# Optimization experiments

Hardware: AMD Instinct MI355X
Metric: run time of the kernel (lower is better)

Reference implementation:

```python
import jax, jax.numpy as jnp
import numpy as np

B, L, DIM = 2, 2048, 768
NH, HD = 12, 64  # num_heads, head_dim; NH*HD == dim_attn == 768


def setup_inputs() -> dict:
    key = jax.random.key(0)
    ks = jax.random.split(key, 7)
    x = jax.random.normal(ks[0], (B, L, DIM), dtype=jnp.float32)
    pos_bias = jax.random.normal(ks[1], (1, NH, L, L), dtype=jnp.float32)
    Wq = jax.random.normal(ks[2], (DIM, DIM), dtype=jnp.float32) * 0.02
    Wk = jax.random.normal(ks[3], (DIM, DIM), dtype=jnp.float32) * 0.02
    Wv = jax.random.normal(ks[4], (DIM, DIM), dtype=jnp.float32) * 0.02
    Wo = jax.random.normal(ks[5], (DIM, DIM), dtype=jnp.float32) * 0.02
    mask = jax.random.randint(ks[6], (B, L), 0, 2, dtype=jnp.int32)
    return {"x": x, "pos_bias": pos_bias, "Wq": Wq, "Wk": Wk, "Wv": Wv,
            "Wo": Wo, "mask": mask}


def reference(x, pos_bias, Wq, Wk, Wv, Wo, mask):
    b, l, _ = x.shape
    # q/k/v projections (torch Linear: x @ W.T), split into heads
    q = (x @ Wq.T).reshape(b, l, NH, HD)
    k = (x @ Wk.T).reshape(b, l, NH, HD)
    v = (x @ Wv.T).reshape(b, l, NH, HD)
    # additive bias [B, H, Lq, Lk]: pos_bias broadcast + key mask -> -inf
    neg_inf = jnp.finfo(x.dtype).min
    attn_bias = jnp.broadcast_to(pos_bias, (b, NH, l, l))
    attn_bias = jnp.where(mask[:, None, None, :] == 0, neg_inf, attn_bias)
    # T5-style attention: NO 1/sqrt(d) scaling
    scores = jnp.einsum('binc,bjnc->bnij', q, k) + attn_bias
    attn = jax.nn.softmax(scores.astype(jnp.float32), axis=-1).astype(x.dtype)
    out = jnp.einsum('bnij,bjnc->binc', attn, v).reshape(b, l, NH * HD)
    return out @ Wo.T
```

## Files before the change

kernel.cpp:

```cpp
#include <hip/hip_runtime.h>
#include <math.h>

#define Bq 2
#define Lq 2048
#define DIMq 768
#define NHq 12
#define HDq 64

typedef __attribute__((ext_vector_type(8))) short short8;
typedef __attribute__((ext_vector_type(4))) short short4v;
typedef __attribute__((ext_vector_type(4))) float float4v;

static __device__ __forceinline__ short f2bf(float f) {
    union { float f; unsigned u; } v; v.f = f;
    unsigned r = (v.u + 0x7FFF + ((v.u >> 16) & 1)) >> 16;
    return (short)r;
}

__global__ __launch_bounds__(256)
void to_bf16(const float* __restrict__ x,  const float* __restrict__ wq,
             const float* __restrict__ wk, const float* __restrict__ wv,
             const float* __restrict__ wo,
             short* __restrict__ xb, short* __restrict__ wqb,
             short* __restrict__ wkb, short* __restrict__ wvb,
             short* __restrict__ wob)
{
    int blk = blockIdx.x;
    const float* s; short* d; int off;
    if      (blk <  768) { s = x;  d = xb;  off = blk * 1024; }
    else if (blk <  912) { s = wq; d = wqb; off = (blk -  768) * 1024; }
    else if (blk < 1056) { s = wk; d = wkb; off = (blk -  912) * 1024; }
    else if (blk < 1200) { s = wv; d = wvb; off = (blk - 1056) * 1024; }
    else                 { s = wo; d = wob; off = (blk - 1200) * 1024; }
    const float4* s4 = (const float4*)s;
    short4v* d4 = (short4v*)d;
#pragma unroll
    for (int i = 0; i < 4; ++i) {
        int idx = off + threadIdx.x + i * 256;
        float4 v = s4[idx];
        short4v o;
        o[0] = f2bf(v.x); o[1] = f2bf(v.y); o[2] = f2bf(v.z); o[3] = f2bf(v.w);
        d4[idx] = o;
    }
}

__global__ __launch_bounds__(256, 2)
void gemm_bf16(const short* __restrict__ A,
               const short* __restrict__ W0, const short* __restrict__ W1,
               const short* __restrict__ W2,
               short* __restrict__ D0, short* __restrict__ D1,
               short* __restrict__ D2, float* __restrict__ DF, int mode)
{
    const int z = blockIdx.z;
    const short* W = (z == 0) ? W0 : ((z == 1) ? W1 : W2);
    short* DH = (z == 0) ? D0 : ((z == 1) ? D1 : D2);

    __shared__ __align__(16) short Xs[64][72];
    __shared__ __align__(16) short Ws[64][72];

    const int tid  = threadIdx.x;
    const int wave = tid >> 6;
    const int lane = tid & 63;
    const int col  = lane & 15;
    const int quad = lane >> 4;
    const int m0 = blockIdx.y * 64, n0 = blockIdx.x * 64;

    float4v acc[4];
#pragma unroll
    for (int nt = 0; nt < 4; ++nt) acc[nt] = (float4v){0.f, 0.f, 0.f, 0.f};

    for (int k0 = 0; k0 < DIMq; k0 += 64) {
        __syncthreads();
#pragma unroll
        for (int i = 0; i < 2; ++i) {
            int idx = tid + i * 256;
            int mm = idx >> 3, ch = idx & 7;
            *(short8*)&Xs[mm][ch * 8] =
                *(const short8*)&A[(size_t)(m0 + mm) * DIMq + k0 + ch * 8];
            *(short8*)&Ws[mm][ch * 8] =
                *(const short8*)&W[(size_t)(n0 + mm) * DIMq + k0 + ch * 8];
        }
        __syncthreads();
#pragma unroll
        for (int kk = 0; kk < 2; ++kk) {
            short8 a = *(const short8*)&Xs[wave * 16 + col][kk * 32 + quad * 8];
#pragma unroll
            for (int nt = 0; nt < 4; ++nt) {
                short8 bfr = *(const short8*)&Ws[nt * 16 + col][kk * 32 + quad * 8];
                acc[nt] = __builtin_amdgcn_mfma_f32_16x16x32_bf16(a, bfr, acc[nt], 0, 0, 0);
            }
        }
    }

#pragma unroll
    for (int reg = 0; reg < 4; ++reg) {
        int m = m0 + wave * 16 + quad * 4 + reg;
#pragma unroll
        for (int nt = 0; nt < 4; ++nt) {
            int n = n0 + 16 * nt + col;
            if (mode == 1) {
                int b = m >> 11, l = m & 2047, h = n >> 6, c = n & 63;
                DH[(((size_t)(b * NHq + h)) * Lq + l) * HDq + c] = f2bf(acc[nt][reg]);
            } else {
                DF[(size_t)m * DIMq + n] = acc[nt][reg];
            }
        }
    }
}

__global__ __launch_bounds__(256, 2)
void attn_fwd_mfma(const short* __restrict__ Qh, const short* __restrict__ Kh,
                   const short* __restrict__ Vh, const float* __restrict__ pos_bias,
                   const int* __restrict__ mask, short* __restrict__ AO)
{
    const int qt = blockIdx.x;
    const int h  = blockIdx.y;
    const int b  = blockIdx.z;
    const short* Q = Qh + ((size_t)(b * NHq + h)) * Lq * HDq;
    const short* K = Kh + ((size_t)(b * NHq + h)) * Lq * HDq;
    const short* V = Vh + ((size_t)(b * NHq + h)) * Lq * HDq;
    const int* mk = mask + (size_t)b * Lq;

    __shared__ __align__(16) short Ks[64][72];
    __shared__ __align__(16) short Vt[64][72];
    __shared__ __align__(16) short Ps[64][72];

    const int tid  = threadIdx.x;
    const int wave = tid >> 6;
    const int lane = tid & 63;
    const int col  = lane & 15;
    const int quad = lane >> 4;

    short8 qa[2];
    {
        const short* qrow = Q + (size_t)(qt * 64 + wave * 16 + col) * HDq;
        qa[0] = *(const short8*)&qrow[quad * 8];
        qa[1] = *(const short8*)&qrow[32 + quad * 8];
    }

    const float* brow = pos_bias + (size_t)h * Lq * Lq
                      + (size_t)(qt * 64 + wave * 16 + quad * 4) * Lq + col;

    float bcur[4][4], bnxt[4][4];
    auto prefetch = [&](int kt, float (&bb)[4][4]) {
#pragma unroll
        for (int nt = 0; nt < 4; ++nt) {
            int mval = mk[kt * 64 + col + 16 * nt];
            float fm = (mval == 0) ? -1e30f : 0.0f;
#pragma unroll
            for (int reg = 0; reg < 4; ++reg)
                bb[nt][reg] = brow[(size_t)reg * Lq + kt * 64 + 16 * nt] + fm;
        }
    };
    prefetch(0, bcur);

    float4v Oacc[4];
    float m_run[4], l_run[4];
#pragma unroll
    for (int nt = 0; nt < 4; ++nt) Oacc[nt] = (float4v){0.f, 0.f, 0.f, 0.f};
#pragma unroll
    for (int r = 0; r < 4; ++r) { m_run[r] = -1e30f; l_run[r] = 0.f; }

    for (int kt = 0; kt < Lq / 64; ++kt) {
        __syncthreads();
        const short* Kt = K + (size_t)kt * 64 * HDq;
        const short* Vg = V + (size_t)kt * 64 * HDq;
#pragma unroll
        for (int i = 0; i < 2; ++i) {
            int idx = tid + i * 256;
            int key = idx >> 3, ch = idx & 7;
            *(short8*)&Ks[key][ch * 8] = *(const short8*)&Kt[key * HDq + ch * 8];
        }
        {
            int key = tid & 63, hg = tid >> 6;
#pragma unroll
            for (int i = 0; i < 2; ++i) {
                int c = hg + i * 4;
                short8 vv = *(const short8*)&Vg[key * HDq + c * 8];
#pragma unroll
                for (int j = 0; j < 8; ++j)
                    Vt[c * 8 + j][key] = vv[j];
            }
        }
        if (kt + 1 < Lq / 64) prefetch(kt + 1, bnxt);
        __syncthreads();

        float4v S[4];
#pragma unroll
        for (int nt = 0; nt < 4; ++nt) S[nt] = (float4v){0.f, 0.f, 0.f, 0.f};
#pragma unroll
        for (int kk = 0; kk < 2; ++kk) {
#pragma unroll
            for (int nt = 0; nt < 4; ++nt) {
                short8 bfr = *(const short8*)&Ks[nt * 16 + col][kk * 32 + quad * 8];
                S[nt] = __builtin_amdgcn_mfma_f32_16x16x32_bf16(qa[kk], bfr, S[nt], 0, 0, 0);
            }
        }

        float sc[4][4];
#pragma unroll
        for (int nt = 0; nt < 4; ++nt)
#pragma unroll
            for (int reg = 0; reg < 4; ++reg)
                sc[nt][reg] = S[nt][reg] + bcur[nt][reg];
        float tm[4];
#pragma unroll
        for (int reg = 0; reg < 4; ++reg) {
            tm[reg] = fmaxf(fmaxf(sc[0][reg], sc[1][reg]),
                            fmaxf(sc[2][reg], sc[3][reg]));
#pragma unroll
            for (int off = 1; off < 16; off <<= 1)
                tm[reg] = fmaxf(tm[reg], __shfl_xor(tm[reg], off, 64));
        }
        float alpha[4], ps[4];
#pragma unroll
        for (int reg = 0; reg < 4; ++reg) {
            float mn = fmaxf(m_run[reg], tm[reg]);
            alpha[reg] = __expf(m_run[reg] - mn);
            m_run[reg] = mn;
            ps[reg] = 0.f;
        }
#pragma unroll
        for (int nt = 0; nt < 4; ++nt)
#pragma unroll
            for (int reg = 0; reg < 4; ++reg) {
                float p = __expf(sc[nt][reg] - m_run[reg]);
                sc[nt][reg] = p;
                ps[reg] += p;
            }
#pragma unroll
        for (int reg = 0; reg < 4; ++reg) {
#pragma unroll
            for (int off = 1; off < 16; off <<= 1)
                ps[reg] += __shfl_xor(ps[reg], off, 64);
            l_run[reg] = l_run[reg] * alpha[reg] + ps[reg];
        }
#pragma unroll
        for (int nt = 0; nt < 4; ++nt)
#pragma unroll
            for (int reg = 0; reg < 4; ++reg)
                Ps[wave * 16 + quad * 4 + reg][col + 16 * nt] = f2bf(sc[nt][reg]);
#pragma unroll
        for (int nt = 0; nt < 4; ++nt)
#pragma unroll
            for (int reg = 0; reg < 4; ++reg)
                Oacc[nt][reg] *= alpha[reg];
        __syncthreads();

#pragma unroll
        for (int kk = 0; kk < 2; ++kk) {
            short8 pa = *(const short8*)&Ps[wave * 16 + col][kk * 32 + quad * 8];
#pragma unroll
            for (int nt = 0; nt < 4; ++nt) {
                short8 vb = *(const short8*)&Vt[nt * 16 + col][kk * 32 + quad * 8];
                Oacc[nt] = __builtin_amdgcn_mfma_f32_16x16x32_bf16(pa, vb, Oacc[nt], 0, 0, 0);
            }
        }
#pragma unroll
        for (int nt = 0; nt < 4; ++nt)
#pragma unroll
            for (int reg = 0; reg < 4; ++reg)
                bcur[nt][reg] = bnxt[nt][reg];
    }

    short* aorow = AO + ((size_t)b * Lq + qt * 64 + wave * 16 + quad * 4) * DIMq
                 + h * HDq + col;
#pragma unroll
    for (int reg = 0; reg < 4; ++reg) {
        float inv = 1.0f / l_run[reg];
#pragma unroll
        for (int nt = 0; nt < 4; ++nt)
            aorow[(size_t)reg * DIMq + 16 * nt] = f2bf(Oacc[nt][reg] * inv);
    }
}

extern "C" void kernel_launch(void* const* d_in, const int* in_sizes, int n_in,
                              void* d_out, int out_size, void* d_ws, size_t ws_size,
                              hipStream_t stream) {
    const float* x        = (const float*)d_in[0];
    const float* pos_bias = (const float*)d_in[1];
    const float* Wq       = (const float*)d_in[2];
    const float* Wk       = (const float*)d_in[3];
    const float* Wv       = (const float*)d_in[4];
    const float* Wo       = (const float*)d_in[5];
    const int*   mask     = (const int*)d_in[6];
    float* out = (float*)d_out;

    const size_t nX = (size_t)Bq * Lq * DIMq;
    const size_t nW = (size_t)DIMq * DIMq;
    short* xb  = (short*)d_ws;
    short* wqb = xb  + nX;
    short* wkb = wqb + nW;
    short* wvb = wkb + nW;
    short* wob = wvb + nW;
    short* Qh  = wob + nW;
    short* Kh  = Qh  + nX;
    short* Vh  = Kh  + nX;
    short* AOb = Vh  + nX;

    dim3 blk(256);
    hipLaunchKernelGGL(to_bf16, dim3(1344), blk, 0, stream,
                       x, Wq, Wk, Wv, Wo, xb, wqb, wkb, wvb, wob);

    hipLaunchKernelGGL(gemm_bf16, dim3(DIMq / 64, (Bq * Lq) / 64, 3), blk, 0, stream,
                       xb, wqb, wkb, wvb, Qh, Kh, Vh, (float*)nullptr, 1);

    hipLaunchKernelGGL(attn_fwd_mfma, dim3(Lq / 64, NHq, Bq), blk, 0, stream,
                       Qh, Kh, Vh, pos_bias, mask, AOb);

    hipLaunchKernelGGL(gemm_bf16, dim3(DIMq / 64, (Bq * Lq) / 64, 1), blk, 0, stream,
                       AOb, wob, wob, wob, (short*)nullptr, (short*)nullptr,
                       (short*)nullptr, out, 0);
}
```

Baseline: 426.0 us.

## Rewrite GEMM and attention with direct global-to-LDS loads and pre-swizzled K/V layouts

Replaces the 64x64 GEMM with a 128x128 tiled GEMM that fuses the QKV projections into one launch and loads tiles straight from global memory into XOR-swizzled LDS. The QKV epilogue writes K and V in pre-swizzled, pre-transposed 32-key blocks, so the attention kernel can stage them with global_load_lds instead of transposing V through registers. Attention now uses 32-key tiles with double-buffered LDS staging of K, V and the bias, keeps the mask in LDS, and raises the occupancy target. The aim is to cut LDS transpose work, register-staged loads and global bias latency, at the cost of more complex layouts and relying on the direct-to-LDS load path.

```diff
diff --git a/kernel.cpp b/kernel.cpp
--- a/kernel.cpp
+++ b/kernel.cpp
@@ -10,6 +10,10 @@
 typedef __attribute__((ext_vector_type(8))) short short8;
 typedef __attribute__((ext_vector_type(4))) short short4v;
 typedef __attribute__((ext_vector_type(4))) float float4v;
+
+#define GL2LDS(g, l) __builtin_amdgcn_global_load_lds( \
+    (const __attribute__((address_space(1))) unsigned int*)(g), \
+    (__attribute__((address_space(3))) unsigned int*)(l), 16, 0, 0)
 
 static __device__ __forceinline__ short f2bf(float f) {
     union { float f; unsigned u; } v; v.f = f;
@@ -45,183 +49,186 @@
 }
 
 __global__ __launch_bounds__(256, 2)
-void gemm_bf16(const short* __restrict__ A,
-               const short* __restrict__ W0, const short* __restrict__ W1,
-               const short* __restrict__ W2,
-               short* __restrict__ D0, short* __restrict__ D1,
-               short* __restrict__ D2, float* __restrict__ DF, int mode)
+void gemm128(const short* __restrict__ A, const short* __restrict__ W,
+             short* __restrict__ Qg, short* __restrict__ Ktg,
+             short* __restrict__ Vtg, float* __restrict__ OutF, int mode)
 {
-    const int z = blockIdx.z;
-    const short* W = (z == 0) ? W0 : ((z == 1) ? W1 : W2);
-    short* DH = (z == 0) ? D0 : ((z == 1) ? D1 : D2);
-
-    __shared__ __align__(16) short Xs[64][72];
-    __shared__ __align__(16) short Ws[64][72];
-
-    const int tid  = threadIdx.x;
-    const int wave = tid >> 6;
-    const int lane = tid & 63;
-    const int col  = lane & 15;
-    const int quad = lane >> 4;
-    const int m0 = blockIdx.y * 64, n0 = blockIdx.x * 64;
-
-    float4v acc[4];
-#pragma unroll
-    for (int nt = 0; nt < 4; ++nt) acc[nt] = (float4v){0.f, 0.f, 0.f, 0.f};
+    __shared__ __align__(16) short As[128 * 64];
+    __shared__ __align__(16) short Bs[128 * 64];
+    const int tid = threadIdx.x;
+    const int wave = tid >> 6, lane = tid & 63;
+    const int col = lane & 15, quad = lane >> 4;
+    const int m0 = blockIdx.y * 128, n0 = blockIdx.x * 128;
+    const int mw = (wave & 1) * 64, nw = (wave >> 1) * 64;
+    const int lr8 = lane >> 3, lc8 = lane & 7;
+
+    float4v acc[4][4];
+#pragma unroll
+    for (int it = 0; it < 4; ++it)
+#pragma unroll
+        for (int nt = 0; nt < 4; ++nt) acc[it][nt] = (float4v){0.f, 0.f, 0.f, 0.f};
 
     for (int k0 = 0; k0 < DIMq; k0 += 64) {
+        if (k0) __syncthreads();
+#pragma unroll
+        for (int i = 0; i < 4; ++i) {
+            int issue = wave * 4 + i;
+            int r = issue * 8 + lr8;
+            int c = lc8 ^ (r & 7);
+            GL2LDS(A + (size_t)(m0 + r) * DIMq + k0 + c * 8, &As[issue * 512]);
+            GL2LDS(W + (size_t)(n0 + r) * DIMq + k0 + c * 8, &Bs[issue * 512]);
+        }
         __syncthreads();
 #pragma unroll
-        for (int i = 0; i < 2; ++i) {
-            int idx = tid + i * 256;
-            int mm = idx >> 3, ch = idx & 7;
-            *(short8*)&Xs[mm][ch * 8] =
-                *(const short8*)&A[(size_t)(m0 + mm) * DIMq + k0 + ch * 8];
-            *(short8*)&Ws[mm][ch * 8] =
-                *(const short8*)&W[(size_t)(n0 + mm) * DIMq + k0 + ch * 8];
-        }
-        __syncthreads();
-#pragma unroll
         for (int kk = 0; kk < 2; ++kk) {
-            short8 a = *(const short8*)&Xs[wave * 16 + col][kk * 32 + quad * 8];
+            short8 a[4], bfr[4];
+#pragma unroll
+            for (int it = 0; it < 4; ++it) {
+                int r = mw + it * 16 + col;
+                a[it] = *(const short8*)&As[r * 64 + (((kk * 4 + quad) ^ (r & 7)) * 8)];
+            }
 #pragma unroll
             for (int nt = 0; nt < 4; ++nt) {
-                short8 bfr = *(const short8*)&Ws[nt * 16 + col][kk * 32 + quad * 8];
-                acc[nt] = __builtin_amdgcn_mfma_f32_16x16x32_bf16(a, bfr, acc[nt], 0, 0, 0);
-            }
-        }
-    }
-
-#pragma unroll
-    for (int reg = 0; reg < 4; ++reg) {
-        int m = m0 + wave * 16 + quad * 4 + reg;
-#pragma unroll
-        for (int nt = 0; nt < 4; ++nt) {
-            int n = n0 + 16 * nt + col;
-            if (mode == 1) {
-                int b = m >> 11, l = m & 2047, h = n >> 6, c = n & 63;
-                DH[(((size_t)(b * NHq + h)) * Lq + l) * HDq + c] = f2bf(acc[nt][reg]);
-            } else {
-                DF[(size_t)m * DIMq + n] = acc[nt][reg];
-            }
-        }
-    }
-}
-
-__global__ __launch_bounds__(256, 2)
-void attn_fwd_mfma(const short* __restrict__ Qh, const short* __restrict__ Kh,
-                   const short* __restrict__ Vh, const float* __restrict__ pos_bias,
-                   const int* __restrict__ mask, short* __restrict__ AO)
+                int r = nw + nt * 16 + col;
+                bfr[nt] = *(const short8*)&Bs[r * 64 + (((kk * 4 + quad) ^ (r & 7)) * 8)];
+            }
+#pragma unroll
+            for (int it = 0; it < 4; ++it)
+#pragma unroll
+                for (int nt = 0; nt < 4; ++nt)
+                    acc[it][nt] = __builtin_amdgcn_mfma_f32_16x16x32_bf16(
+                        a[it], bfr[nt], acc[it][nt], 0, 0, 0);
+        }
+    }
+
+    if (mode == 0) {
+#pragma unroll
+        for (int it = 0; it < 4; ++it)
+#pragma unroll
+            for (int reg = 0; reg < 4; ++reg) {
+                float* orow = OutF + (size_t)(m0 + mw + it * 16 + quad * 4 + reg) * DIMq
+                            + n0 + nw + col;
+#pragma unroll
+                for (int nt = 0; nt < 4; ++nt) orow[nt * 16] = acc[it][nt][reg];
+            }
+    } else {
+        const int mat = n0 / 768;
+        const int nbase = n0 - mat * 768 + nw;
+#pragma unroll
+        for (int it = 0; it < 4; ++it)
+#pragma unroll
+            for (int reg = 0; reg < 4; ++reg) {
+                int m = m0 + mw + it * 16 + quad * 4 + reg;
+                int bb = m >> 11, l = m & 2047;
+#pragma unroll
+                for (int nt = 0; nt < 4; ++nt) {
+                    int nloc = nbase + nt * 16 + col;
+                    int hh = nloc >> 6, c = nloc & 63;
+                    size_t bh = (size_t)(bb * NHq + hh);
+                    short v = f2bf(acc[it][nt][reg]);
+                    if (mat == 0) {
+                        Qg[(bh * Lq + l) * HDq + c] = v;
+                    } else if (mat == 1) {
+                        Ktg[(bh * 64 + (l >> 5)) * 2048 + (l & 31) * 64
+                            + (((c >> 3) ^ (l & 7)) * 8) + (c & 7)] = v;
+                    } else {
+                        Vtg[(bh * 64 + (l >> 5)) * 2048 + c * 32
+                            + ((((l & 31) >> 3) + (c >> 1)) & 3) * 8 + (l & 7)] = v;
+                    }
+                }
+            }
+    }
+}
+
+__global__ __launch_bounds__(256, 3)
+void attn_fwd2(const short* __restrict__ Qg, const short* __restrict__ Ktg,
+               const short* __restrict__ Vtg, const float* __restrict__ pos_bias,
+               const int* __restrict__ mask, short* __restrict__ AO)
 {
-    const int qt = blockIdx.x;
-    const int h  = blockIdx.y;
-    const int b  = blockIdx.z;
-    const short* Q = Qh + ((size_t)(b * NHq + h)) * Lq * HDq;
-    const short* K = Kh + ((size_t)(b * NHq + h)) * Lq * HDq;
-    const short* V = Vh + ((size_t)(b * NHq + h)) * Lq * HDq;
-    const int* mk = mask + (size_t)b * Lq;
-
-    __shared__ __align__(16) short Ks[64][72];
-    __shared__ __align__(16) short Vt[64][72];
-    __shared__ __align__(16) short Ps[64][72];
-
-    const int tid  = threadIdx.x;
-    const int wave = tid >> 6;
-    const int lane = tid & 63;
-    const int col  = lane & 15;
-    const int quad = lane >> 4;
-
-    short8 qa[2];
-    {
-        const short* qrow = Q + (size_t)(qt * 64 + wave * 16 + col) * HDq;
-        qa[0] = *(const short8*)&qrow[quad * 8];
-        qa[1] = *(const short8*)&qrow[32 + quad * 8];
-    }
-
-    const float* brow = pos_bias + (size_t)h * Lq * Lq
-                      + (size_t)(qt * 64 + wave * 16 + quad * 4) * Lq + col;
-
-    float bcur[4][4], bnxt[4][4];
-    auto prefetch = [&](int kt, float (&bb)[4][4]) {
-#pragma unroll
-        for (int nt = 0; nt < 4; ++nt) {
-            int mval = mk[kt * 64 + col + 16 * nt];
-            float fm = (mval == 0) ? -1e30f : 0.0f;
+    __shared__ __align__(16) short Ks[2][2048];
+    __shared__ __align__(16) short Vt[2][2048];
+    __shared__ __align__(16) float Bsh[2][2048];
+    __shared__ __align__(16) float mAll[Lq];
+    __shared__ __align__(16) short Ps[64][40];
+
+    const int qt = blockIdx.x, h = blockIdx.y, b = blockIdx.z;
+    const int bh = b * NHq + h;
+    const int tid = threadIdx.x;
+    const int wave = tid >> 6, lane = tid & 63;
+    const int col = lane & 15, quad = lane >> 4;
+    const int lr8 = lane >> 3, lc8 = lane & 7;
+
+    const short* Kb = Ktg + (size_t)bh * 64 * 2048;
+    const short* Vb = Vtg + (size_t)bh * 64 * 2048;
+    const float* Bb = pos_bias + (size_t)h * Lq * Lq + (size_t)(qt * 64) * Lq;
+    const int* mk = mask + b * Lq;
+
+    for (int i = tid; i < Lq; i += 256) mAll[i] = mk[i] ? 0.0f : -1e38f;
+
+    const short* qrow = Qg + ((size_t)bh * Lq + qt * 64 + wave * 16 + col) * HDq;
+    const short8 qa0 = *(const short8*)&qrow[quad * 8];
+    const short8 qa1 = *(const short8*)&qrow[32 + quad * 8];
+
+    auto stage = [&](int kt, int buf) {
+        GL2LDS(Kb + (size_t)kt * 2048 + wave * 512 + lane * 8, &Ks[buf][wave * 512]);
+        GL2LDS(Vb + (size_t)kt * 2048 + wave * 512 + lane * 8, &Vt[buf][wave * 512]);
+#pragma unroll
+        for (int j2 = 0; j2 < 2; ++j2) {
+            int j = wave * 2 + j2;
+            GL2LDS(Bb + (size_t)(j * 8 + lr8) * Lq + kt * 32 + lc8 * 4,
+                   &Bsh[buf][j * 256]);
+        }
+    };
+
+    stage(0, 0);
+
+    float4v O[4];
+    float m_run[4], l_run[4];
+#pragma unroll
+    for (int nt = 0; nt < 4; ++nt) O[nt] = (float4v){0.f, 0.f, 0.f, 0.f};
+#pragma unroll
+    for (int r = 0; r < 4; ++r) { m_run[r] = -1e37f; l_run[r] = 0.f; }
+
+    __syncthreads();
+
+    const int brow = wave * 16 + quad * 4;
+    for (int kt = 0; kt < 64; ++kt) {
+        const int cur = kt & 1;
+        if (kt + 1 < 64) stage(kt + 1, cur ^ 1);
+
+        float4v S[2];
+#pragma unroll
+        for (int nt = 0; nt < 2; ++nt) {
+            S[nt] = (float4v){0.f, 0.f, 0.f, 0.f};
+            int key = nt * 16 + col;
+            short8 kb0 = *(const short8*)&Ks[cur][key * 64 + ((quad ^ (key & 7)) * 8)];
+            short8 kb1 = *(const short8*)&Ks[cur][key * 64 + (((4 + quad) ^ (key & 7)) * 8)];
+            S[nt] = __builtin_amdgcn_mfma_f32_16x16x32_bf16(qa0, kb0, S[nt], 0, 0, 0);
+            S[nt] = __builtin_amdgcn_mfma_f32_16x16x32_bf16(qa1, kb1, S[nt], 0, 0, 0);
+        }
+
+        float sc[2][4];
+#pragma unroll
+        for (int nt = 0; nt < 2; ++nt) {
+            float fm = mAll[kt * 32 + col + 16 * nt];
 #pragma unroll
             for (int reg = 0; reg < 4; ++reg)
-                bb[nt][reg] = brow[(size_t)reg * Lq + kt * 64 + 16 * nt] + fm;
-        }
-    };
-    prefetch(0, bcur);
-
-    float4v Oacc[4];
-    float m_run[4], l_run[4];
-#pragma unroll
-    for (int nt = 0; nt < 4; ++nt) Oacc[nt] = (float4v){0.f, 0.f, 0.f, 0.f};
-#pragma unroll
-    for (int r = 0; r < 4; ++r) { m_run[r] = -1e30f; l_run[r] = 0.f; }
-
-    for (int kt = 0; kt < Lq / 64; ++kt) {
-        __syncthreads();
-        const short* Kt = K + (size_t)kt * 64 * HDq;
-        const short* Vg = V + (size_t)kt * 64 * HDq;
-#pragma unroll
-        for (int i = 0; i < 2; ++i) {
-            int idx = tid + i * 256;
-            int key = idx >> 3, ch = idx & 7;
-            *(short8*)&Ks[key][ch * 8] = *(const short8*)&Kt[key * HDq + ch * 8];
-        }
-        {
-            int key = tid & 63, hg = tid >> 6;
-#pragma unroll
-            for (int i = 0; i < 2; ++i) {
-                int c = hg + i * 4;
-                short8 vv = *(const short8*)&Vg[key * HDq + c * 8];
-#pragma unroll
-                for (int j = 0; j < 8; ++j)
-                    Vt[c * 8 + j][key] = vv[j];
-            }
-        }
-        if (kt + 1 < Lq / 64) prefetch(kt + 1, bnxt);
-        __syncthreads();
-
-        float4v S[4];
-#pragma unroll
-        for (int nt = 0; nt < 4; ++nt) S[nt] = (float4v){0.f, 0.f, 0.f, 0.f};
-#pragma unroll
-        for (int kk = 0; kk < 2; ++kk) {
-#pragma unroll
-            for (int nt = 0; nt < 4; ++nt) {
-                short8 bfr = *(const short8*)&Ks[nt * 16 + col][kk * 32 + quad * 8];
-                S[nt] = __builtin_amdgcn_mfma_f32_16x16x32_bf16(qa[kk], bfr, S[nt], 0, 0, 0);
-            }
-        }
-
-        float sc[4][4];
-#pragma unroll
-        for (int nt = 0; nt < 4; ++nt)
-#pragma unroll
-            for (int reg = 0; reg < 4; ++reg)
-                sc[nt][reg] = S[nt][reg] + bcur[nt][reg];
-        float tm[4];
+                sc[nt][reg] = S[nt][reg] + Bsh[cur][(brow + reg) * 32 + col + 16 * nt] + fm;
+        }
+        float tm[4], alpha[4], ps[4];
 #pragma unroll
         for (int reg = 0; reg < 4; ++reg) {
-            tm[reg] = fmaxf(fmaxf(sc[0][reg], sc[1][reg]),
-                            fmaxf(sc[2][reg], sc[3][reg]));
+            tm[reg] = fmaxf(sc[0][reg], sc[1][reg]);
 #pragma unroll
             for (int off = 1; off < 16; off <<= 1)
                 tm[reg] = fmaxf(tm[reg], __shfl_xor(tm[reg], off, 64));
-        }
-        float alpha[4], ps[4];
-#pragma unroll
-        for (int reg = 0; reg < 4; ++reg) {
             float mn = fmaxf(m_run[reg], tm[reg]);
             alpha[reg] = __expf(m_run[reg] - mn);
             m_run[reg] = mn;
             ps[reg] = 0.f;
         }
 #pragma unroll
-        for (int nt = 0; nt < 4; ++nt)
+        for (int nt = 0; nt < 2; ++nt)
 #pragma unroll
             for (int reg = 0; reg < 4; ++reg) {
                 float p = __expf(sc[nt][reg] - m_run[reg]);
@@ -236,41 +243,35 @@
             l_run[reg] = l_run[reg] * alpha[reg] + ps[reg];
         }
 #pragma unroll
+        for (int nt = 0; nt < 2; ++nt)
+#pragma unroll
+            for (int reg = 0; reg < 4; ++reg)
+                Ps[brow + reg][col + 16 * nt] = f2bf(sc[nt][reg]);
+#pragma unroll
         for (int nt = 0; nt < 4; ++nt)
 #pragma unroll
             for (int reg = 0; reg < 4; ++reg)
-                Ps[wave * 16 + quad * 4 + reg][col + 16 * nt] = f2bf(sc[nt][reg]);
-#pragma unroll
-        for (int nt = 0; nt < 4; ++nt)
-#pragma unroll
-            for (int reg = 0; reg < 4; ++reg)
-                Oacc[nt][reg] *= alpha[reg];
+                O[nt][reg] *= alpha[reg];
+        asm volatile("s_waitcnt lgkmcnt(0)" ::: "memory");
+
+        short8 pa = *(const short8*)&Ps[wave * 16 + col][quad * 8];
+#pragma unroll
+        for (int nt = 0; nt < 4; ++nt) {
+            int hd = nt * 16 + col;
+            short8 vb = *(const short8*)&Vt[cur][hd * 32 + (((quad + (hd >> 1)) & 3) * 8)];
+            O[nt] = __builtin_amdgcn_mfma_f32_16x16x32_bf16(pa, vb, O[nt], 0, 0, 0);
+        }
+
         __syncthreads();
-
-#pragma unroll
-        for (int kk = 0; kk < 2; ++kk) {
-            short8 pa = *(const short8*)&Ps[wave * 16 + col][kk * 32 + quad * 8];
-#pragma unroll
-            for (int nt = 0; nt < 4; ++nt) {
-                short8 vb = *(const short8*)&Vt[nt * 16 + col][kk * 32 + quad * 8];
-                Oacc[nt] = __builtin_amdgcn_mfma_f32_16x16x32_bf16(pa, vb, Oacc[nt], 0, 0, 0);
-            }
-        }
-#pragma unroll
-        for (int nt = 0; nt < 4; ++nt)
-#pragma unroll
-            for (int reg = 0; reg < 4; ++reg)
-                bcur[nt][reg] = bnxt[nt][reg];
-    }
-
-    short* aorow = AO + ((size_t)b * Lq + qt * 64 + wave * 16 + quad * 4) * DIMq
-                 + h * HDq + col;
+    }
+
+    short* aorow = AO + ((size_t)b * Lq + qt * 64 + brow) * DIMq + h * HDq + col;
 #pragma unroll
     for (int reg = 0; reg < 4; ++reg) {
         float inv = 1.0f / l_run[reg];
 #pragma unroll
         for (int nt = 0; nt < 4; ++nt)
-            aorow[(size_t)reg * DIMq + 16 * nt] = f2bf(Oacc[nt][reg] * inv);
+            aorow[(size_t)reg * DIMq + 16 * nt] = f2bf(O[nt][reg] * inv);
     }
 }
 
@@ -288,27 +289,25 @@
 
     const size_t nX = (size_t)Bq * Lq * DIMq;
     const size_t nW = (size_t)DIMq * DIMq;
-    short* xb  = (short*)d_ws;
-    short* wqb = xb  + nX;
-    short* wkb = wqb + nW;
-    short* wvb = wkb + nW;
-    short* wob = wvb + nW;
-    short* Qh  = wob + nW;
-    short* Kh  = Qh  + nX;
-    short* Vh  = Kh  + nX;
-    short* AOb = Vh  + nX;
+    short* xb   = (short*)d_ws;
+    short* wqkv = xb + nX;
+    short* wob  = wqkv + 3 * nW;
+    short* Qg   = wob + nW;
+    short* Ktg  = Qg + nX;
+    short* Vtg  = Ktg + nX;
+    short* AOb  = Vtg + nX;
 
     dim3 blk(256);
     hipLaunchKernelGGL(to_bf16, dim3(1344), blk, 0, stream,
-                       x, Wq, Wk, Wv, Wo, xb, wqb, wkb, wvb, wob);
-
-    hipLaunchKernelGGL(gemm_bf16, dim3(DIMq / 64, (Bq * Lq) / 64, 3), blk, 0, stream,
-                       xb, wqb, wkb, wvb, Qh, Kh, Vh, (float*)nullptr, 1);
-
-    hipLaunchKernelGGL(attn_fwd_mfma, dim3(Lq / 64, NHq, Bq), blk, 0, stream,
-                       Qh, Kh, Vh, pos_bias, mask, AOb);
-
-    hipLaunchKernelGGL(gemm_bf16, dim3(DIMq / 64, (Bq * Lq) / 64, 1), blk, 0, stream,
-                       AOb, wob, wob, wob, (short*)nullptr, (short*)nullptr,
+                       x, Wq, Wk, Wv, Wo, xb, wqkv, wqkv + nW, wqkv + 2 * nW, wob);
+
+    hipLaunchKernelGGL(gemm128, dim3(2304 / 128, (Bq * Lq) / 128), blk, 0, stream,
+                       xb, wqkv, Qg, Ktg, Vtg, (float*)nullptr, 1);
+
+    hipLaunchKernelGGL(attn_fwd2, dim3(Lq / 64, NHq, Bq), blk, 0, stream,
+                       Qg, Ktg, Vtg, pos_bias, mask, AOb);
+
+    hipLaunchKernelGGL(gemm128, dim3(DIMq / 128, (Bq * Lq) / 128), blk, 0, stream,
+                       AOb, wob, (short*)nullptr, (short*)nullptr,
                        (short*)nullptr, out, 0);
 }
```

Measured after the change: 431.9 us. Within noise of the previous version (+1.4%).
